# Performance work log

Measured on AMD Instinct MI355X. Metric: run time of the kernel, lower is better.

Reference implementation:

```python
import jax, jax.numpy as jnp
import numpy as np

B, T, D_IN, D_ENC, D_H = 16384, 60, 3, 64, 128


def setup_inputs() -> dict:
    key = jax.random.key(0)
    ks = jax.random.split(key, 10)
    s_enc = 1.0 / np.sqrt(D_IN)
    s_lstm = 1.0 / np.sqrt(D_H)
    s_dec = 1.0 / np.sqrt(D_H)
    return {
        "x": jax.random.normal(ks[0], (B, D_IN), dtype=jnp.float32),
        "W_enc": jax.random.uniform(ks[1], (D_ENC, D_IN), jnp.float32, -s_enc, s_enc),
        "b_enc": jax.random.uniform(ks[2], (D_ENC,), jnp.float32, -s_enc, s_enc),
        "W_ih": jax.random.uniform(ks[3], (4 * D_H, D_ENC), jnp.float32, -s_lstm, s_lstm),
        "W_hh": jax.random.uniform(ks[4], (4 * D_H, D_H), jnp.float32, -s_lstm, s_lstm),
        "b_ih": jax.random.uniform(ks[5], (4 * D_H,), jnp.float32, -s_lstm, s_lstm),
        "b_hh": jax.random.uniform(ks[6], (4 * D_H,), jnp.float32, -s_lstm, s_lstm),
        "W_dec": jax.random.uniform(ks[7], (1, D_H), jnp.float32, -s_dec, s_dec),
        "b_dec": jax.random.uniform(ks[8], (1,), jnp.float32, -s_dec, s_dec),
    }


def _forward(x, W_enc, b_enc, W_ih, W_hh, b_ih, b_hh, W_dec, b_dec):
    encoded = x @ W_enc.T + b_enc  # [B, 64]
    # Input to LSTM is identical at every timestep -> precompute Wx projection once.
    xp = encoded @ W_ih.T + b_ih + b_hh  # [B, 4*H], PyTorch gate order i,f,g,o
    h0 = jnp.zeros((x.shape[0], D_H), x.dtype)
    c0 = jnp.zeros((x.shape[0], D_H), x.dtype)

    def step(carry, _):
        h, c = carry
        gates = xp + h @ W_hh.T  # [B, 4*H]
        i, f, g, o = jnp.split(gates, 4, axis=-1)
        i = jax.nn.sigmoid(i)
        f = jax.nn.sigmoid(f)
        g = jnp.tanh(g)
        o = jax.nn.sigmoid(o)
        c = f * c + i * g
        h = o * jnp.tanh(c)
        return (h, c), h

    (_, _), hs = jax.lax.scan(step, (h0, c0), None, length=T)  # hs: [T, B, H]
    lstm_out = jnp.transpose(hs, (1, 0, 2))  # [B, T, H]
    out = (lstm_out @ W_dec.T + b_dec)[..., 0]  # [B, T]
    return jax.nn.sigmoid(out)


def reference(x, W_enc, b_enc, W_ih, W_hh, b_ih, b_hh, W_dec, b_dec):
    return _forward(x, W_enc, b_enc, W_ih, W_hh, b_ih, b_hh, W_dec, b_dec)
```

## Files before the change

### kernel.cpp

```cpp
#include <hip/hip_runtime.h>

#define T_STEPS 60
#define HID 128
#define ROWS 16
#define NBLK (16384 / ROWS)

typedef __attribute__((ext_vector_type(8))) short short8;
typedef __attribute__((ext_vector_type(4))) float f32x4;

#define K1 1.44269504088896340736f

__device__ __forceinline__ unsigned short f2bf(float f) {
  unsigned u = __float_as_uint(f);
  return (unsigned short)((u + 0x7fffu + ((u >> 16) & 1u)) >> 16);
}
__device__ __forceinline__ float sigm(float x) {
  return __builtin_amdgcn_rcpf(1.0f + __expf(-x));
}
template <int CTRL>
__device__ __forceinline__ float dppadd(float x) {
  int y = __builtin_amdgcn_update_dpp(0, __builtin_bit_cast(int, x), CTRL, 0xf,
                                      0xf, false);
  return x + __builtin_bit_cast(float, y);
}

#define HB0 0
#define HB1 4096
#define PART 8192
#define WSTRIDE 968
#define LDS_BYTES (PART + 8 * WSTRIDE * 4)

__global__ __launch_bounds__(512, 2) void lstm_fused(
    const float* __restrict__ x, const float* __restrict__ W_enc,
    const float* __restrict__ b_enc, const float* __restrict__ W_ih,
    const float* __restrict__ W_hh, const float* __restrict__ b_ih,
    const float* __restrict__ b_hh, const float* __restrict__ W_dec,
    const float* __restrict__ b_dec, float* __restrict__ out) {
  __shared__ __align__(16) unsigned char lds[LDS_BYTES];

  const int tid = threadIdx.x;
  const int wav = tid >> 6;
  const int lane = tid & 63;
  const int l15 = lane & 15;
  const int l4 = lane >> 4;
  const int u = wav * 16 + l15;
  const int row0 = blockIdx.x * ROWS;

  for (int i = tid; i < 1024; i += 512) ((unsigned*)(lds + HB0))[i] = 0u;

  f32x4 xp4[4];
  {
    float xr0[4], xr1[4], xr2[4];
#pragma unroll
    for (int v = 0; v < 4; ++v) {
      int r = 4 * l4 + v;
      const float* xp_ = x + (size_t)(row0 + r) * 3;
      xr0[v] = xp_[0];
      xr1[v] = xp_[1];
      xr2[v] = xp_[2];
    }
#pragma unroll
    for (int gt = 0; gt < 4; ++gt) {
      float bias = b_ih[gt * 128 + u] + b_hh[gt * 128 + u];
#pragma unroll
      for (int v = 0; v < 4; ++v) xp4[gt][v] = bias;
    }
    const f32x4* wr0 = (const f32x4*)(W_ih + (size_t)u * 64);
    const f32x4* wr1 = (const f32x4*)(W_ih + (size_t)(128 + u) * 64);
    const f32x4* wr2 = (const f32x4*)(W_ih + (size_t)(256 + u) * 64);
    const f32x4* wr3 = (const f32x4*)(W_ih + (size_t)(384 + u) * 64);
    for (int e4 = 0; e4 < 16; ++e4) {
      f32x4 w0 = wr0[e4], w1 = wr1[e4], w2 = wr2[e4], w3 = wr3[e4];
#pragma unroll
      for (int j = 0; j < 4; ++j) {
        int e = e4 * 4 + j;
        float we0 = W_enc[e * 3], we1 = W_enc[e * 3 + 1], we2 = W_enc[e * 3 + 2];
        float be = b_enc[e];
#pragma unroll
        for (int v = 0; v < 4; ++v) {
          float ev = fmaf(we0, xr0[v], fmaf(we1, xr1[v], fmaf(we2, xr2[v], be)));
          xp4[0][v] = fmaf(w0[j], ev, xp4[0][v]);
          xp4[1][v] = fmaf(w1[j], ev, xp4[1][v]);
          xp4[2][v] = fmaf(w2[j], ev, xp4[2][v]);
          xp4[3][v] = fmaf(w3[j], ev, xp4[3][v]);
        }
      }
    }
#pragma unroll
    for (int gt = 0; gt < 4; ++gt) {
      float s = (gt == 2) ? (-2.0f * K1) : (-K1);
#pragma unroll
      for (int v = 0; v < 4; ++v) xp4[gt][v] *= s;
    }
  }

  short8 bw[4][4];
#pragma unroll
  for (int gt = 0; gt < 4; ++gt) {
    float s = (gt == 2) ? (-2.0f * K1) : (-K1);
#pragma unroll
    for (int kt = 0; kt < 4; ++kt) {
      const float* p = W_hh + (size_t)(gt * 128 + u) * HID + kt * 32 + 8 * l4;
      short8 f;
#pragma unroll
      for (int j = 0; j < 8; ++j) f[j] = (short)f2bf(s * p[j]);
      bw[gt][kt] = f;
    }
  }

  float ct[4];
#pragma unroll
  for (int v = 0; v < 4; ++v) ct[v] = 0.0f;

  const unsigned swzA =
      (((unsigned)(l15 & 7)) << 4) ^ (((unsigned)(l15 & 8)) << 2);
  unsigned rdA[4];
#pragma unroll
  for (int kt = 0; kt < 4; ++kt)
    rdA[kt] = ((unsigned)(l15 * 256 + l4 * 16 + kt * 64)) ^ swzA;
  unsigned wrA[4];
#pragma unroll
  for (int v = 0; v < 4; ++v) {
    unsigned rr = (unsigned)(4 * l4 + v);
    wrA[v] = (rr * 256 + (unsigned)u * 2) ^ ((rr & 7u) << 4) ^ ((rr & 8u) << 2);
  }
  const float wdu = W_dec[u];
  const unsigned ptByte = (unsigned)(wav * WSTRIDE + 4 * l4) * 4;
  const float kneg = -2.0f * K1;
  const float kpos = 2.0f * K1;

  __syncthreads();

#define STEP(RB, WB, tcur)                                                     \
  {                                                                            \
    f32x4 acc[4];                                                              \
    {                                                                          \
      short8 af = *(const short8*)(lds + (RB) + rdA[0]);                       \
      _Pragma("unroll") for (int gt = 0; gt < 4; ++gt) acc[gt] =               \
          __builtin_amdgcn_mfma_f32_16x16x32_bf16(af, bw[gt][0], xp4[gt],      \
                                                  0, 0, 0);                    \
    }                                                                          \
    _Pragma("unroll") for (int kt = 1; kt < 4; ++kt) {                         \
      short8 af = *(const short8*)(lds + (RB) + rdA[kt]);                      \
      _Pragma("unroll") for (int gt = 0; gt < 4; ++gt) acc[gt] =               \
          __builtin_amdgcn_mfma_f32_16x16x32_bf16(af, bw[gt][kt], acc[gt],     \
                                                  0, 0, 0);                    \
    }                                                                          \
    f32x4 pz;                                                                  \
    _Pragma("unroll") for (int v = 0; v < 4; ++v) {                            \
      float ea = __builtin_amdgcn_exp2f(acc[0][v]);                            \
      float ef = __builtin_amdgcn_exp2f(acc[1][v]);                            \
      float eg = __builtin_amdgcn_exp2f(acc[2][v]);                            \
      float eo = __builtin_amdgcn_exp2f(acc[3][v]);                            \
      float A = 1.0f + ea, F = 1.0f + ef, G = 1.0f + eg, Bo = 1.0f + eo;       \
      float AG = A * G;                                                        \
      float r = __builtin_amdgcn_rcpf(F * AG);                                 \
      float tt = fmaf(kpos, eg, kneg);                                         \
      float num = fmaf(ct[v], AG, tt * F);                                     \
      float cn = num * r;                                                      \
      ct[v] = cn;                                                              \
      float ec = __builtin_amdgcn_exp2f(cn);                                   \
      float r2 = __builtin_amdgcn_rcpf(Bo * (1.0f + ec));                      \
      float h = (1.0f - ec) * r2;                                              \
      *(unsigned short*)(lds + (WB) + wrA[v]) = f2bf(h);                       \
      pz[v] = h * wdu;                                                         \
    }                                                                          \
           \
    _Pragma("unroll") for (int v = 0; v < 4; ++v) pz[v] =                      \
        dppadd<0x140>(dppadd<0x141>(dppadd<0x4E>(dppadd<0xB1>(pz[v]))));       \
    if (l15 == 0)                                                              \
      *(f32x4*)(lds + PART + ptByte + (unsigned)(tcur)*64) = pz;               \
    __syncthreads();                                                           \
  }

  for (int t = 0; t < T_STEPS; t += 2) {
    STEP(HB0, HB1, t)
    STEP(HB1, HB0, t + 1)
  }
#undef STEP

  const float bdec = b_dec[0];
  const float* partf = (const float*)(lds + PART);
  for (int i = tid; i < 16 * T_STEPS; i += 512) {
    int r = i / T_STEPS, t = i - r * T_STEPS;
    float s = 0.0f;
#pragma unroll
    for (int w = 0; w < 8; ++w) s += partf[w * WSTRIDE + t * 16 + r];
    out[(size_t)(row0 + r) * T_STEPS + t] = sigm(s + bdec);
  }
}

extern "C" void kernel_launch(void* const* d_in, const int* in_sizes, int n_in,
                              void* d_out, int out_size, void* d_ws, size_t ws_size,
                              hipStream_t stream) {
  const float* x = (const float*)d_in[0];
  const float* W_enc = (const float*)d_in[1];
  const float* b_enc = (const float*)d_in[2];
  const float* W_ih = (const float*)d_in[3];
  const float* W_hh = (const float*)d_in[4];
  const float* b_ih = (const float*)d_in[5];
  const float* b_hh = (const float*)d_in[6];
  const float* W_dec = (const float*)d_in[7];
  const float* b_dec = (const float*)d_in[8];
  float* out = (float*)d_out;

  dim3 grid(NBLK);
  dim3 block(512);
  lstm_fused<<<grid, block, 0, stream>>>(x, W_enc, b_enc, W_ih, W_hh, b_ih, b_hh,
                                         W_dec, b_dec, out);
}
```

Measured before the change: 289.1 us.

## Split LSTM recurrence K-dimension across two wave halves with LDS partial-sum reduction

Doubles the block to 1024 threads and splits the hidden-state K reduction in half, so each wave issues 8 MFMAs per step instead of 16. Partial gate sums go to LDS, and after a barrier each wave reduces and activates one hidden row, so the output reduction no longer needs a final cross-wave pass. The input projection moves from registers to LDS. The cost is a second __syncthreads per step, extra LDS traffic for the partial gates, and a large LDS footprint (about 108 KB) that likely limits resident blocks per CU.

```diff
diff --git a/kernel.cpp b/kernel.cpp
--- a/kernel.cpp
+++ b/kernel.cpp
@@ -24,13 +24,15 @@
   return x + __builtin_bit_cast(float, y);
 }
 
-#define HB0 0
-#define HB1 4096
-#define PART 8192
-#define WSTRIDE 968
-#define LDS_BYTES (PART + 8 * WSTRIDE * 4)
-
-__global__ __launch_bounds__(512, 2) void lstm_fused(
+#define HB 0
+#define PRE 8192
+#define PRE_H 33024
+#define PRE_R 2064
+#define XP 74240
+#define OS 107008
+#define LDS_BYTES 110848
+
+__global__ __launch_bounds__(1024, 4) void lstm_fused(
     const float* __restrict__ x, const float* __restrict__ W_enc,
     const float* __restrict__ b_enc, const float* __restrict__ W_ih,
     const float* __restrict__ W_hh, const float* __restrict__ b_ih,
@@ -43,13 +45,15 @@
   const int lane = tid & 63;
   const int l15 = lane & 15;
   const int l4 = lane >> 4;
-  const int u = wav * 16 + l15;
+  const int ug = wav >> 1;
+  const int half = wav & 1;
+  const int u = ug * 16 + l15;
   const int row0 = blockIdx.x * ROWS;
 
-  for (int i = tid; i < 1024; i += 512) ((unsigned*)(lds + HB0))[i] = 0u;
-
-  f32x4 xp4[4];
+  if (tid < 1024) ((unsigned*)(lds + HB))[tid] = 0u;
+
   {
+    f32x4 xp4[4];
     float xr0[4], xr1[4], xr2[4];
 #pragma unroll
     for (int v = 0; v < 4; ++v) {
@@ -65,129 +69,162 @@
 #pragma unroll
       for (int v = 0; v < 4; ++v) xp4[gt][v] = bias;
     }
-    const f32x4* wr0 = (const f32x4*)(W_ih + (size_t)u * 64);
-    const f32x4* wr1 = (const f32x4*)(W_ih + (size_t)(128 + u) * 64);
-    const f32x4* wr2 = (const f32x4*)(W_ih + (size_t)(256 + u) * 64);
-    const f32x4* wr3 = (const f32x4*)(W_ih + (size_t)(384 + u) * 64);
+    const f32x4* wp0 = (const f32x4*)(W_ih + (size_t)u * 64);
+    const f32x4* wp1 = (const f32x4*)(W_ih + (size_t)(128 + u) * 64);
+    const f32x4* wp2 = (const f32x4*)(W_ih + (size_t)(256 + u) * 64);
+    const f32x4* wp3 = (const f32x4*)(W_ih + (size_t)(384 + u) * 64);
     for (int e4 = 0; e4 < 16; ++e4) {
-      f32x4 w0 = wr0[e4], w1 = wr1[e4], w2 = wr2[e4], w3 = wr3[e4];
-#pragma unroll
-      for (int j = 0; j < 4; ++j) {
-        int e = e4 * 4 + j;
+      f32x4 w0 = wp0[e4], w1 = wp1[e4], w2 = wp2[e4], w3 = wp3[e4];
+#pragma unroll
+      for (int jj = 0; jj < 4; ++jj) {
+        int e = e4 * 4 + jj;
         float we0 = W_enc[e * 3], we1 = W_enc[e * 3 + 1], we2 = W_enc[e * 3 + 2];
         float be = b_enc[e];
 #pragma unroll
         for (int v = 0; v < 4; ++v) {
           float ev = fmaf(we0, xr0[v], fmaf(we1, xr1[v], fmaf(we2, xr2[v], be)));
-          xp4[0][v] = fmaf(w0[j], ev, xp4[0][v]);
-          xp4[1][v] = fmaf(w1[j], ev, xp4[1][v]);
-          xp4[2][v] = fmaf(w2[j], ev, xp4[2][v]);
-          xp4[3][v] = fmaf(w3[j], ev, xp4[3][v]);
+          xp4[0][v] = fmaf(w0[jj], ev, xp4[0][v]);
+          xp4[1][v] = fmaf(w1[jj], ev, xp4[1][v]);
+          xp4[2][v] = fmaf(w2[jj], ev, xp4[2][v]);
+          xp4[3][v] = fmaf(w3[jj], ev, xp4[3][v]);
         }
       }
     }
-#pragma unroll
-    for (int gt = 0; gt < 4; ++gt) {
-      float s = (gt == 2) ? (-2.0f * K1) : (-K1);
-#pragma unroll
-      for (int v = 0; v < 4; ++v) xp4[gt][v] *= s;
-    }
-  }
-
-  short8 bw[4][4];
+    if (half == 0) {
+#pragma unroll
+      for (int gt = 0; gt < 4; ++gt) {
+        float s = (gt == 2) ? (-2.0f * K1) : (-K1);
+#pragma unroll
+        for (int v = 0; v < 4; ++v) xp4[gt][v] *= s;
+        *(f32x4*)(lds + XP + (unsigned)gt * 8192 +
+                  (unsigned)(ug * 64 + lane) * 16) = xp4[gt];
+      }
+    }
+  }
+
+  short8 bw[4][2];
 #pragma unroll
   for (int gt = 0; gt < 4; ++gt) {
     float s = (gt == 2) ? (-2.0f * K1) : (-K1);
 #pragma unroll
-    for (int kt = 0; kt < 4; ++kt) {
+    for (int j = 0; j < 2; ++j) {
+      int kt = 2 * half + j;
       const float* p = W_hh + (size_t)(gt * 128 + u) * HID + kt * 32 + 8 * l4;
       short8 f;
 #pragma unroll
-      for (int j = 0; j < 8; ++j) f[j] = (short)f2bf(s * p[j]);
-      bw[gt][kt] = f;
-    }
-  }
-
-  float ct[4];
-#pragma unroll
-  for (int v = 0; v < 4; ++v) ct[v] = 0.0f;
+      for (int jj = 0; jj < 8; ++jj) f[jj] = (short)f2bf(s * p[jj]);
+      bw[gt][j] = f;
+    }
+  }
+
+  float ct0 = 0.0f, ct1 = 0.0f;
 
   const unsigned swzA =
       (((unsigned)(l15 & 7)) << 4) ^ (((unsigned)(l15 & 8)) << 2);
-  unsigned rdA[4];
-#pragma unroll
-  for (int kt = 0; kt < 4; ++kt)
-    rdA[kt] = ((unsigned)(l15 * 256 + l4 * 16 + kt * 64)) ^ swzA;
-  unsigned wrA[4];
-#pragma unroll
-  for (int v = 0; v < 4; ++v) {
-    unsigned rr = (unsigned)(4 * l4 + v);
-    wrA[v] = (rr * 256 + (unsigned)u * 2) ^ ((rr & 7u) << 4) ^ ((rr & 8u) << 2);
-  }
-  const float wdu = W_dec[u];
-  const unsigned ptByte = (unsigned)(wav * WSTRIDE + 4 * l4) * 4;
+  const unsigned rdA =
+      ((unsigned)(l15 * 256 + l4 * 16 + half * 128)) ^ swzA;
+  const unsigned rdB =
+      ((unsigned)(l15 * 256 + l4 * 16 + half * 128 + 64)) ^ swzA;
+  const unsigned pwr = PRE + (unsigned)half * PRE_H +
+                       (unsigned)(4 * l4) * PRE_R + (unsigned)(ug * 16 + l15) * 16;
+  const unsigned xpAddr = XP + (unsigned)(ug * 64 + lane) * 16;
+  const int rw = wav;
+  const unsigned prd0 = PRE + (unsigned)rw * PRE_R + (unsigned)lane * 16;
+  const unsigned prd1 = prd0 + 1024;
+  const unsigned swzR =
+      (((unsigned)(rw & 7)) << 4) ^ (((unsigned)(rw & 8)) << 2);
+  const unsigned hw0 = ((unsigned)(rw * 256 + 2 * lane)) ^ swzR;
+  const unsigned hw1 = ((unsigned)(rw * 256 + 2 * lane + 128)) ^ swzR;
+  const float wd0 = W_dec[lane];
+  const float wd1 = W_dec[lane + 64];
+  const unsigned osA = OS + (unsigned)(rw * T_STEPS) * 4;
   const float kneg = -2.0f * K1;
   const float kpos = 2.0f * K1;
 
+  unsigned hbR = HB, hbW = HB + 4096;
+
   __syncthreads();
 
-#define STEP(RB, WB, tcur)                                                     \
+#define ACT(S, CT, H)                                                          \
   {                                                                            \
-    f32x4 acc[4];                                                              \
-    {                                                                          \
-      short8 af = *(const short8*)(lds + (RB) + rdA[0]);                       \
-      _Pragma("unroll") for (int gt = 0; gt < 4; ++gt) acc[gt] =               \
-          __builtin_amdgcn_mfma_f32_16x16x32_bf16(af, bw[gt][0], xp4[gt],      \
-                                                  0, 0, 0);                    \
-    }                                                                          \
-    _Pragma("unroll") for (int kt = 1; kt < 4; ++kt) {                         \
-      short8 af = *(const short8*)(lds + (RB) + rdA[kt]);                      \
-      _Pragma("unroll") for (int gt = 0; gt < 4; ++gt) acc[gt] =               \
-          __builtin_amdgcn_mfma_f32_16x16x32_bf16(af, bw[gt][kt], acc[gt],     \
-                                                  0, 0, 0);                    \
-    }                                                                          \
-    f32x4 pz;                                                                  \
-    _Pragma("unroll") for (int v = 0; v < 4; ++v) {                            \
-      float ea = __builtin_amdgcn_exp2f(acc[0][v]);                            \
-      float ef = __builtin_amdgcn_exp2f(acc[1][v]);                            \
-      float eg = __builtin_amdgcn_exp2f(acc[2][v]);                            \
-      float eo = __builtin_amdgcn_exp2f(acc[3][v]);                            \
-      float A = 1.0f + ea, F = 1.0f + ef, G = 1.0f + eg, Bo = 1.0f + eo;       \
-      float AG = A * G;                                                        \
-      float r = __builtin_amdgcn_rcpf(F * AG);                                 \
-      float tt = fmaf(kpos, eg, kneg);                                         \
-      float num = fmaf(ct[v], AG, tt * F);                                     \
-      float cn = num * r;                                                      \
-      ct[v] = cn;                                                              \
-      float ec = __builtin_amdgcn_exp2f(cn);                                   \
-      float r2 = __builtin_amdgcn_rcpf(Bo * (1.0f + ec));                      \
-      float h = (1.0f - ec) * r2;                                              \
-      *(unsigned short*)(lds + (WB) + wrA[v]) = f2bf(h);                       \
-      pz[v] = h * wdu;                                                         \
-    }                                                                          \
-           \
-    _Pragma("unroll") for (int v = 0; v < 4; ++v) pz[v] =                      \
-        dppadd<0x140>(dppadd<0x141>(dppadd<0x4E>(dppadd<0xB1>(pz[v]))));       \
-    if (l15 == 0)                                                              \
-      *(f32x4*)(lds + PART + ptByte + (unsigned)(tcur)*64) = pz;               \
-    __syncthreads();                                                           \
-  }
-
-  for (int t = 0; t < T_STEPS; t += 2) {
-    STEP(HB0, HB1, t)
-    STEP(HB1, HB0, t + 1)
-  }
-#undef STEP
+    float ea = __builtin_amdgcn_exp2f(S[0]);                                   \
+    float ef = __builtin_amdgcn_exp2f(S[1]);                                   \
+    float eg = __builtin_amdgcn_exp2f(S[2]);                                   \
+    float eo = __builtin_amdgcn_exp2f(S[3]);                                   \
+    float A = 1.0f + ea, F = 1.0f + ef, G = 1.0f + eg, Bo = 1.0f + eo;         \
+    float AG = A * G;                                                          \
+    float r = __builtin_amdgcn_rcpf(F * AG);                                   \
+    float tt = fmaf(kpos, eg, kneg);                                           \
+    float num = fmaf(CT, AG, tt * F);                                          \
+    float cn = num * r;                                                        \
+    CT = cn;                                                                   \
+    float ec = __builtin_amdgcn_exp2f(cn);                                     \
+    float r2 = __builtin_amdgcn_rcpf(Bo * (1.0f + ec));                        \
+    H = (1.0f - ec) * r2;                                                      \
+  }
+
+#pragma clang loop unroll(disable)
+  for (int t = 0; t < T_STEPS; ++t) {
+    short8 afa = *(const short8*)(lds + hbR + rdA);
+    short8 afb = *(const short8*)(lds + hbR + rdB);
+    f32x4 a0, a1, a2, a3;
+    if (half == 0) {
+      a0 = __builtin_amdgcn_mfma_f32_16x16x32_bf16(
+          afa, bw[0][0], *(const f32x4*)(lds + xpAddr), 0, 0, 0);
+      a1 = __builtin_amdgcn_mfma_f32_16x16x32_bf16(
+          afa, bw[1][0], *(const f32x4*)(lds + xpAddr + 8192), 0, 0, 0);
+      a2 = __builtin_amdgcn_mfma_f32_16x16x32_bf16(
+          afa, bw[2][0], *(const f32x4*)(lds + xpAddr + 16384), 0, 0, 0);
+      a3 = __builtin_amdgcn_mfma_f32_16x16x32_bf16(
+          afa, bw[3][0], *(const f32x4*)(lds + xpAddr + 24576), 0, 0, 0);
+    } else {
+      f32x4 z = {};
+      a0 = __builtin_amdgcn_mfma_f32_16x16x32_bf16(afa, bw[0][0], z, 0, 0, 0);
+      a1 = __builtin_amdgcn_mfma_f32_16x16x32_bf16(afa, bw[1][0], z, 0, 0, 0);
+      a2 = __builtin_amdgcn_mfma_f32_16x16x32_bf16(afa, bw[2][0], z, 0, 0, 0);
+      a3 = __builtin_amdgcn_mfma_f32_16x16x32_bf16(afa, bw[3][0], z, 0, 0, 0);
+    }
+    a0 = __builtin_amdgcn_mfma_f32_16x16x32_bf16(afb, bw[0][1], a0, 0, 0, 0);
+    a1 = __builtin_amdgcn_mfma_f32_16x16x32_bf16(afb, bw[1][1], a1, 0, 0, 0);
+    a2 = __builtin_amdgcn_mfma_f32_16x16x32_bf16(afb, bw[2][1], a2, 0, 0, 0);
+    a3 = __builtin_amdgcn_mfma_f32_16x16x32_bf16(afb, bw[3][1], a3, 0, 0, 0);
+#pragma unroll
+    for (int v = 0; v < 4; ++v) {
+      f32x4 q;
+      q[0] = a0[v]; q[1] = a1[v]; q[2] = a2[v]; q[3] = a3[v];
+      *(f32x4*)(lds + pwr + (unsigned)v * PRE_R) = q;
+    }
+    __syncthreads();
+
+    f32x4 sa = *(const f32x4*)(lds + prd0);
+    {
+      f32x4 t2 = *(const f32x4*)(lds + prd0 + PRE_H);
+      sa += t2;
+    }
+    f32x4 sb = *(const f32x4*)(lds + prd1);
+    {
+      f32x4 t2 = *(const f32x4*)(lds + prd1 + PRE_H);
+      sb += t2;
+    }
+    float h0, h1;
+    ACT(sa, ct0, h0)
+    ACT(sb, ct1, h1)
+    *(unsigned short*)(lds + hbW + hw0) = f2bf(h0);
+    *(unsigned short*)(lds + hbW + hw1) = f2bf(h1);
+    float pz = fmaf(h0, wd0, h1 * wd1);
+    pz = dppadd<0x140>(dppadd<0x141>(dppadd<0x4E>(dppadd<0xB1>(pz))));
+    pz += __shfl_xor(pz, 16, 64);
+    pz += __shfl_xor(pz, 32, 64);
+    if (lane == 0) *(float*)(lds + osA + (unsigned)t * 4) = pz;
+    __syncthreads();
+    unsigned tmp = hbR; hbR = hbW; hbW = tmp;
+  }
+#undef ACT
 
   const float bdec = b_dec[0];
-  const float* partf = (const float*)(lds + PART);
-  for (int i = tid; i < 16 * T_STEPS; i += 512) {
-    int r = i / T_STEPS, t = i - r * T_STEPS;
-    float s = 0.0f;
-#pragma unroll
-    for (int w = 0; w < 8; ++w) s += partf[w * WSTRIDE + t * 16 + r];
-    out[(size_t)(row0 + r) * T_STEPS + t] = sigm(s + bdec);
-  }
+  const float* OSf = (const float*)(lds + OS);
+  if (tid < ROWS * T_STEPS)
+    out[(size_t)row0 * T_STEPS + tid] = sigm(OSf[tid] + bdec);
 }
 
 extern "C" void kernel_launch(void* const* d_in, const int* in_sizes, int n_in,
@@ -205,7 +242,7 @@
   float* out = (float*)d_out;
 
   dim3 grid(NBLK);
-  dim3 block(512);
+  dim3 block(1024);
   lstm_fused<<<grid, block, 0, stream>>>(x, W_enc, b_enc, W_ih, W_hh, b_ih, b_hh,
                                          W_dec, b_dec, out);
 }
```

Result: slower. 462.5 us (+60.0%).
